# Optimization experiments

Hardware: AMD Instinct MI355X
Metric: run time of the kernel (lower is better)

## Reference

```python
import jax, jax.numpy as jnp
import numpy as np

NEG_SLOPE = 0.2


def _gcn_conv(x, edge_index, W, b):
    # Standard GCNConv: y = D^-1/2 (A + I) D^-1/2 (x W) + b
    N = x.shape[0]
    loop = jnp.arange(N, dtype=edge_index.dtype)
    src = jnp.concatenate([edge_index[0], loop])  # [E+N]
    dst = jnp.concatenate([edge_index[1], loop])  # [E+N]
    deg = jax.ops.segment_sum(jnp.ones_like(dst, dtype=x.dtype), dst, num_segments=N)
    dinv = jnp.where(deg > 0, jax.lax.rsqrt(deg), 0.0)
    norm = dinv[src] * dinv[dst]                  # [E+N]
    h = x @ W                                     # [N, out] dense GEMM
    msg = h[src] * norm[:, None]                  # irregular gather, [E+N, out]
    agg = jax.ops.segment_sum(msg, dst, num_segments=N)  # irregular scatter
    return agg + b


def setup_inputs() -> dict:
    key = jax.random.key(0)
    ks = jax.random.split(key, 5)
    N, E, d_in, d_hid = 50000, 800000, 256, 512
    s = lambda fan_in, fan_out: np.sqrt(6.0 / (fan_in + fan_out))
    return {
        "x": jax.random.normal(ks[0], (N, d_in), dtype=jnp.float32),
        "edge_index": jax.random.randint(ks[1], (2, E), 0, N, dtype=jnp.int64),
        "W_gcn": jax.random.uniform(ks[2], (d_in, d_hid), jnp.float32, -s(d_in, d_hid), s(d_in, d_hid)),
        "b_gcn": jnp.zeros((d_hid,), jnp.float32),
        "W2": jax.random.uniform(ks[3], (d_hid, d_hid), jnp.float32, -s(d_hid, d_hid), s(d_hid, d_hid)),
        "b2": jnp.zeros((d_hid,), jnp.float32),
        "W_out": jax.random.uniform(ks[4], (d_hid, 1), jnp.float32, -s(d_hid, 1), s(d_hid, 1)),
        "b_out": jnp.zeros((1,), jnp.float32),
    }


def reference(x, edge_index, W_gcn, b_gcn, W2, b2, W_out, b_out):
    h = _gcn_conv(x, edge_index, W_gcn, b_gcn)           # [N, 512]
    h = jax.nn.leaky_relu(h, NEG_SLOPE)
    h = jax.nn.leaky_relu(h @ W2 + b2, NEG_SLOPE)        # [N, 512]
    return h @ W_out + b_out                             # [N, 1]
```

## Files before the change

### kernel.cpp

```cpp
#include <hip/hip_runtime.h>

#define D_IN  256
#define D_HID 512
#define NEG_SLOPE 0.2f
#define SCAN_CHUNK 2048

typedef __attribute__((ext_vector_type(8))) short short8;
typedef __attribute__((ext_vector_type(4))) float floatx4;

__device__ __forceinline__ unsigned short f2bf(float f) {
    unsigned int u = __float_as_uint(f);
    u += 0x7fffu + ((u >> 16) & 1u);
    return (unsigned short)(u >> 16);
}
__device__ __forceinline__ float bf2f(unsigned short u) {
    return __uint_as_float(((unsigned int)u) << 16);
}

__device__ __forceinline__ int eidx(const void* ei, long pos, int is64) {
    return is64 ? (int)((const long long*)ei)[pos] : ((const int*)ei)[pos];
}

__global__ __launch_bounds__(256) void k_init(int* __restrict__ deg, int N,
                                              const unsigned int* __restrict__ ei,
                                              int npairs, int* flag,
                                              const float* __restrict__ b_out,
                                              float* __restrict__ out,
                                              const float* __restrict__ Wa,
                                              unsigned short* __restrict__ Wat,
                                              const float* __restrict__ Wb,
                                              unsigned short* __restrict__ Wbt) {
    __shared__ float tl[64][65];
    int b = blockIdx.x;
    if (b < 96) {
        const float* W; unsigned short* Wt; int K, Nc, tk, tn;
        if (b < 32) { W = Wa; Wt = Wat; K = 256; Nc = 512; tk = b & 3; tn = b >> 2; }
        else { b -= 32; W = Wb; Wt = Wbt; K = 512; Nc = 512; tk = b & 7; tn = b >> 3; }
        int k0 = tk * 64, n0 = tn * 64;
        int c = threadIdx.x & 63;
        int r0 = threadIdx.x >> 6;
#pragma unroll
        for (int i = 0; i < 16; ++i) {
            int r = r0 + i * 4;
            tl[r][c] = W[(long)(k0 + r) * Nc + n0 + c];
        }
        __syncthreads();
#pragma unroll
        for (int i = 0; i < 16; ++i) {
            int r = r0 + i * 4;
            Wt[(long)(n0 + r) * K + k0 + c] = f2bf(tl[c][r]);
        }
        return;
    }
    if (b == 96) {
        __shared__ int nz;
        if (threadIdx.x == 0) nz = 0;
        __syncthreads();
        for (int p = threadIdx.x; p < npairs; p += blockDim.x)
            if (ei[2 * p + 1] != 0) nz = 1;
        __syncthreads();
        if (threadIdx.x == 0) *flag = nz ? 0 : 1;
    }
    int t = (b - 96) * 256 + threadIdx.x;
    if (t < N) { deg[t] = 0; out[t] = b_out[0]; }
}

__global__ void k_deg_count(const void* __restrict__ ei, const int* __restrict__ flag,
                            int* __restrict__ deg, int E) {
    int e = blockIdx.x * blockDim.x + threadIdx.x;
    if (e < E) atomicAdd(&deg[eidx(ei, (long)E + e, *flag)], 1);
}

__global__ __launch_bounds__(256) void k_scan1(const int* __restrict__ deg,
                                               int* __restrict__ bsum, int N) {
    int base = blockIdx.x * SCAN_CHUNK;
    int hi = min(base + SCAN_CHUNK, N);
    int s = 0;
    for (int i = base + threadIdx.x; i < hi; i += 256) s += deg[i];
#pragma unroll
    for (int off = 32; off > 0; off >>= 1) s += __shfl_down(s, off, 64);
    __shared__ int lds[4];
    if ((threadIdx.x & 63) == 0) lds[threadIdx.x >> 6] = s;
    __syncthreads();
    if (threadIdx.x == 0) bsum[blockIdx.x] = lds[0] + lds[1] + lds[2] + lds[3];
}

__global__ __launch_bounds__(256) void k_scan23(const int* __restrict__ deg,
                                                const int* __restrict__ bsum, int NB,
                                                int* __restrict__ offs,
                                                int* __restrict__ cursor,
                                                float* __restrict__ dinv, int N) {
    __shared__ int lds[256];
    int t = threadIdx.x;
    int bbase = 0;
    for (int i = 0; i < NB; ++i) bbase += (i < blockIdx.x) ? bsum[i] : 0;
    if (blockIdx.x == NB - 1 && t == 0) offs[N] = bbase + bsum[NB - 1];
    int base = blockIdx.x * SCAN_CHUNK;
    int lo = base + t * 8;
    int v[8], s = 0;
#pragma unroll
    for (int j = 0; j < 8; ++j) {
        int i = lo + j;
        v[j] = (i < N) ? deg[i] : 0;
        s += v[j];
    }
    lds[t] = s;
    __syncthreads();
    for (int d = 1; d < 256; d <<= 1) {
        int add = (t >= d) ? lds[t - d] : 0;
        __syncthreads();
        lds[t] += add;
        __syncthreads();
    }
    int run = bbase + ((t > 0) ? lds[t - 1] : 0);
#pragma unroll
    for (int j = 0; j < 8; ++j) {
        int i = lo + j;
        if (i < N) {
            offs[i] = run; cursor[i] = run;
            dinv[i] = rsqrtf(1.0f + (float)v[j]);
            run += v[j];
        }
    }
}

__global__ __launch_bounds__(256) void k_prefill(const float* __restrict__ x,
                                                 const float* __restrict__ dinv,
                                                 unsigned short* __restrict__ xb,
                                                 const void* __restrict__ ei,
                                                 const int* __restrict__ flag,
                                                 int* __restrict__ cursor,
                                                 int* __restrict__ esrc,
                                                 int N, int E, int PB) {
    if ((int)blockIdx.x < PB) {
        long t = (long)blockIdx.x * 256 + threadIdx.x;
        long total = (long)N * D_IN / 4;
        if (t >= total) return;
        int row = (int)(t >> 6);
        float s = dinv[row];
        float4 v = *(const float4*)(x + t * 4);
        ushort4 o;
        o.x = f2bf(v.x * s); o.y = f2bf(v.y * s); o.z = f2bf(v.z * s); o.w = f2bf(v.w * s);
        *(ushort4*)(xb + t * 4) = o;
        return;
    }
    int e = (blockIdx.x - PB) * 256 + threadIdx.x;
    if (e >= E) return;
    int is64 = *flag;
    int s = eidx(ei, e, is64), d = eidx(ei, (long)E + e, is64);
    int pos = atomicAdd(&cursor[d], 1);
    esrc[pos] = s;
}

__global__ __launch_bounds__(256) void k_gather(const unsigned short* __restrict__ xb,
                                                const int* __restrict__ offs,
                                                const int* __restrict__ esrc,
                                                const float* __restrict__ dinv,
                                                unsigned short* __restrict__ aggb, int N) {
    int node = blockIdx.x * 4 + (threadIdx.x >> 6);
    if (node >= N) return;
    int lane = threadIdx.x & 63;
    int half = lane >> 5;
    int colofs = (lane & 31) * 8;
    const unsigned short* xbc = xb + colofs;
    float di = dinv[node];

    float a[8];
    {
        short8 v = *(const short8*)(xbc + (long)node * D_IN);
#pragma unroll
        for (int j = 0; j < 8; ++j)
            a[j] = (half == 0) ? bf2f((unsigned short)v[j]) : 0.f;
    }

    int beg = offs[node], end = offs[node + 1];
    int e = beg;
    for (; e + 8 <= end; e += 8) {
        int s0 = esrc[e + half];
        int s1 = esrc[e + 2 + half];
        int s2 = esrc[e + 4 + half];
        int s3 = esrc[e + 6 + half];
        short8 u0 = *(const short8*)(xbc + (long)s0 * D_IN);
        short8 u1 = *(const short8*)(xbc + (long)s1 * D_IN);
        short8 u2 = *(const short8*)(xbc + (long)s2 * D_IN);
        short8 u3 = *(const short8*)(xbc + (long)s3 * D_IN);
#pragma unroll
        for (int j = 0; j < 8; ++j) {
            float t0 = bf2f((unsigned short)u0[j]) + bf2f((unsigned short)u1[j]);
            float t1 = bf2f((unsigned short)u2[j]) + bf2f((unsigned short)u3[j]);
            a[j] += t0 + t1;
        }
    }
    for (; e < end; e += 2) {
        int j0 = e + half;
        int jj = (j0 < end) ? j0 : end - 1;
        int s = esrc[jj];
        float w = (j0 < end) ? 1.f : 0.f;
        short8 u = *(const short8*)(xbc + (long)s * D_IN);
#pragma unroll
        for (int j = 0; j < 8; ++j)
            a[j] += w * bf2f((unsigned short)u[j]);
    }

#pragma unroll
    for (int j = 0; j < 8; ++j) a[j] += __shfl_xor(a[j], 32, 64);

    if (half == 0) {
        short8 o;
#pragma unroll
        for (int j = 0; j < 8; ++j) o[j] = (short)f2bf(a[j] * di);
        *(short8*)(aggb + (long)node * D_IN + colofs) = o;
    }
}

__device__ __forceinline__ void async_cp16(const unsigned short* gp, unsigned short* lp) {
    __builtin_amdgcn_global_load_lds((const __attribute__((address_space(1))) void*)gp,
                                     (__attribute__((address_space(3))) void*)lp, 16, 0, 0);
}

__device__ __forceinline__ void stage_sw64(const unsigned short* src, int strideK,
                                           int rowMax, unsigned short* lds, int tid) {
#pragma unroll
    for (int rr = 0; rr < 4; ++rr) {
        int c = rr * 256 + tid;
        int row = c >> 3;
        int ci = (c & 7) ^ (row & 7);
        if (row > rowMax) row = rowMax;
        async_cp16(src + (long)row * strideK + ci * 8, lds + c * 8);
    }
}

__device__ __forceinline__ bool map_block(int b, int M, int& m0, int& n0) {
    int x = b & 7, slot = b >> 3;
    int mt = x + 8 * (slot >> 2);
    m0 = mt * 128; n0 = (slot & 3) * 128;
    return m0 < M;
}

__global__ __launch_bounds__(256) void k_gemm_bf16(const unsigned short* __restrict__ A,
                                                   const unsigned short* __restrict__ Bt,
                                                   const float* __restrict__ bias,
                                                   unsigned short* __restrict__ C,
                                                   int M, int K) {
    __shared__ __align__(16) unsigned short As[2][128 * 64];
    __shared__ __align__(16) unsigned short Bs[2][128 * 64];
    __shared__ __align__(16) unsigned short Ep[32 * 128];
    const int tid  = threadIdx.x;
    const int lane = tid & 63, wave = tid >> 6;
    int m0, n0;
    if (!map_block(blockIdx.x, M, m0, n0)) return;
    const int r = lane & 15, q = lane >> 4;
    const int xv = r & 7;
    const int wm = (wave & 1) * 64, wn = (wave >> 1) * 64;
    const int band = wm >> 6;
    const int rmA = M - 1 - m0;
    const unsigned short* Ab = A + (long)m0 * K;
    const unsigned short* Bb = Bt + (long)n0 * K;

    floatx4 acc[4][4];
#pragma unroll
    for (int i = 0; i < 4; ++i)
#pragma unroll
        for (int j = 0; j < 4; ++j) acc[i][j] = (floatx4){0.f, 0.f, 0.f, 0.f};

    const int nt = K >> 6;
    stage_sw64(Ab, K, rmA, As[0], tid);
    stage_sw64(Bb, K, 127, Bs[0], tid);
    __syncthreads();
    for (int t = 0; t < nt; ++t) {
        const int cur = t & 1;
        if (t + 1 < nt) {
            stage_sw64(Ab + (t + 1) * 64, K, rmA, As[cur ^ 1], tid);
            stage_sw64(Bb + (t + 1) * 64, K, 127, Bs[cur ^ 1], tid);
        }
#pragma unroll
        for (int s = 0; s < 2; ++s) {
            int slotbase = s * 4 + q;
            short8 af[4], bf[4];
#pragma unroll
            for (int i = 0; i < 4; ++i)
                af[i] = *(const short8*)(As[cur] + (wm + i * 16 + r) * 64 + (slotbase ^ xv) * 8);
#pragma unroll
            for (int j = 0; j < 4; ++j)
                bf[j] = *(const short8*)(Bs[cur] + (wn + j * 16 + r) * 64 + (slotbase ^ xv) * 8);
#pragma unroll
            for (int i = 0; i < 4; ++i)
#pragma unroll
                for (int j = 0; j < 4; ++j)
                    acc[i][j] = __builtin_amdgcn_mfma_f32_16x16x32_bf16(af[i], bf[j], acc[i][j], 0, 0, 0);
        }
        __syncthreads();
    }

    float bv[4];
#pragma unroll
    for (int j = 0; j < 4; ++j) bv[j] = bias[n0 + wn + j * 16 + r];

#pragma unroll
    for (int i = 0; i < 4; ++i) {
#pragma unroll
        for (int j = 0; j < 4; ++j) {
#pragma unroll
            for (int t2 = 0; t2 < 4; ++t2) {
                float v = acc[i][j][t2] + bv[j];
                v = v > 0.f ? v : NEG_SLOPE * v;
                Ep[(band * 16 + q * 4 + t2) * 128 + wn + j * 16 + r] = f2bf(v);
            }
        }
        __syncthreads();
#pragma unroll
        for (int rr = 0; rr < 2; ++rr) {
            int c = rr * 256 + tid;
            int lrow = c >> 4, ccol = c & 15;
            int grow = m0 + (lrow >> 4) * 64 + i * 16 + (lrow & 15);
            if (grow < M) {
                short8 v = *(const short8*)(Ep + lrow * 128 + ccol * 8);
                *(short8*)(C + (long)grow * D_HID + n0 + ccol * 8) = v;
            }
        }
        __syncthreads();
    }
}

__global__ __launch_bounds__(256) void k_gemm2f(const unsigned short* __restrict__ A,
                                                const unsigned short* __restrict__ Bt,
                                                const float* __restrict__ bias,
                                                const float* __restrict__ wout,
                                                float* __restrict__ out,
                                                int M, int K) {
    __shared__ __align__(16) unsigned short As[2][128 * 64];
    __shared__ __align__(16) unsigned short Bs[2][128 * 64];
    const int tid  = threadIdx.x;
    const int lane = tid & 63, wave = tid >> 6;
    int m0, n0;
    if (!map_block(blockIdx.x, M, m0, n0)) return;
    const int r = lane & 15, q = lane >> 4;
    const int xv = r & 7;
    const int wm = (wave & 1) * 64, wn = (wave >> 1) * 64;
    const int rmA = M - 1 - m0;
    const unsigned short* Ab = A + (long)m0 * K;
    const unsigned short* Bb = Bt + (long)n0 * K;

    floatx4 acc[4][4];
#pragma unroll
    for (int i = 0; i < 4; ++i)
#pragma unroll
        for (int j = 0; j < 4; ++j) acc[i][j] = (floatx4){0.f, 0.f, 0.f, 0.f};

    const int nt = K >> 6;
    stage_sw64(Ab, K, rmA, As[0], tid);
    stage_sw64(Bb, K, 127, Bs[0], tid);
    __syncthreads();
    for (int t = 0; t < nt; ++t) {
        const int cur = t & 1;
        if (t + 1 < nt) {
            stage_sw64(Ab + (t + 1) * 64, K, rmA, As[cur ^ 1], tid);
            stage_sw64(Bb + (t + 1) * 64, K, 127, Bs[cur ^ 1], tid);
        }
#pragma unroll
        for (int s = 0; s < 2; ++s) {
            int slotbase = s * 4 + q;
            short8 af[4], bf[4];
#pragma unroll
            for (int i = 0; i < 4; ++i)
                af[i] = *(const short8*)(As[cur] + (wm + i * 16 + r) * 64 + (slotbase ^ xv) * 8);
#pragma unroll
            for (int j = 0; j < 4; ++j)
                bf[j] = *(const short8*)(Bs[cur] + (wn + j * 16 + r) * 64 + (slotbase ^ xv) * 8);
#pragma unroll
            for (int i = 0; i < 4; ++i)
#pragma unroll
                for (int j = 0; j < 4; ++j)
                    acc[i][j] = __builtin_amdgcn_mfma_f32_16x16x32_bf16(af[i], bf[j], acc[i][j], 0, 0, 0);
        }
        __syncthreads();
    }

    float bv[4], wv[4];
#pragma unroll
    for (int j = 0; j < 4; ++j) {
        int col = n0 + wn + j * 16 + r;
        bv[j] = bias[col];
        wv[j] = wout[col];
    }
#pragma unroll
    for (int i = 0; i < 4; ++i) {
#pragma unroll
        for (int t2 = 0; t2 < 4; ++t2) {
            float p = 0.f;
#pragma unroll
            for (int j = 0; j < 4; ++j) {
                float v = acc[i][j][t2] + bv[j];
                v = v > 0.f ? v : NEG_SLOPE * v;
                p += v * wv[j];
            }
            p += __shfl_xor(p, 8, 64);
            p += __shfl_xor(p, 4, 64);
            p += __shfl_xor(p, 2, 64);
            p += __shfl_xor(p, 1, 64);
            if (r == 0) {
                int row = m0 + wm + i * 16 + q * 4 + t2;
                if (row < M) atomicAdd(&out[row], p);
            }
        }
    }
}

extern "C" void kernel_launch(void* const* d_in, const int* in_sizes, int n_in,
                              void* d_out, int out_size, void* d_ws, size_t ws_size,
                              hipStream_t stream) {
    const float* x     = (const float*)d_in[0];
    const void*  ei    = d_in[1];
    const float* W_gcn = (const float*)d_in[2];
    const float* b_gcn = (const float*)d_in[3];
    const float* W2    = (const float*)d_in[4];
    const float* b2    = (const float*)d_in[5];
    const float* W_out = (const float*)d_in[6];
    const float* b_out = (const float*)d_in[7];
    float* out = (float*)d_out;

    const int N = in_sizes[0] / D_IN;
    const int E = in_sizes[1] / 2;
    const int NB = (N + SCAN_CHUNK - 1) / SCAN_CHUNK;

    char* w = (char*)d_ws;
    size_t off = 0;
    auto alloc = [&](size_t bytes) { char* p = w + off; off = (off + bytes + 255) & ~(size_t)255; return p; };
    int*            flag   = (int*)alloc(256);
    float*          dinv   = (float*)alloc((size_t)N * 4);
    int*            deg_i  = (int*)alloc((size_t)N * 4);
    int*            offs   = (int*)alloc((size_t)(N + 1) * 4);
    int*            cursor = (int*)alloc((size_t)N * 4);
    int*            bsum   = (int*)alloc((size_t)NB * 4);
    int*            esrc   = (int*)alloc((size_t)(E + 16) * 4);
    unsigned short* xb     = (unsigned short*)alloc((size_t)N * D_IN * 2);
    unsigned short* aggb   = (unsigned short*)alloc((size_t)N * D_IN * 2);
    unsigned short* h1     = (unsigned short*)alloc((size_t)N * D_HID * 2);
    unsigned short* Wgt    = (unsigned short*)alloc((size_t)D_IN * D_HID * 2);
    unsigned short* W2t    = (unsigned short*)alloc((size_t)D_HID * D_HID * 2);

    int npairs = E < 2048 ? E : 2048;
    int init_blocks = 96 + (N + 255) / 256;
    k_init<<<init_blocks, 256, 0, stream>>>(deg_i, N, (const unsigned int*)ei,
                                            npairs, flag, b_out, out,
                                            W_gcn, Wgt, W2, W2t);

    k_deg_count<<<(E + 255) / 256, 256, 0, stream>>>(ei, flag, deg_i, E);
    k_scan1<<<NB, 256, 0, stream>>>(deg_i, bsum, N);
    k_scan23<<<NB, 256, 0, stream>>>(deg_i, bsum, NB, offs, cursor, dinv, N);

    int PB = (int)(((long)N * D_IN / 4 + 255) / 256);
    int FB = (E + 255) / 256;
    k_prefill<<<PB + FB, 256, 0, stream>>>(x, dinv, xb, ei, flag, cursor, esrc, N, E, PB);

    k_gather<<<(N + 3) / 4, 256, 0, stream>>>(xb, offs, esrc, dinv, aggb, N);

    int mtiles = (N + 127) / 128;
    int gblocks = ((mtiles + 7) / 8) * 8 * 4;
    k_gemm_bf16<<<gblocks, 256, 0, stream>>>(aggb, Wgt, b_gcn, h1, N, D_IN);
    k_gemm2f<<<gblocks, 256, 0, stream>>>(h1, W2t, b2, W_out, out, N, D_HID);
}
```

Baseline: 336.7 us.

## Build CSR from atomic ranks and apply source normalization inside the gather

```diff
diff --git a/kernel.cpp b/kernel.cpp
--- a/kernel.cpp
+++ b/kernel.cpp
@@ -21,7 +21,9 @@
     return is64 ? (int)((const long long*)ei)[pos] : ((const int*)ei)[pos];
 }
 
-__global__ __launch_bounds__(256) void k_init(int* __restrict__ deg, int N,
+__global__ __launch_bounds__(256) void k_init(const float* __restrict__ x,
+                                              unsigned short* __restrict__ xb,
+                                              int* __restrict__ deg, int N,
                                               const unsigned int* __restrict__ ei,
                                               int npairs, int* flag,
                                               const float* __restrict__ b_out,
@@ -29,7 +31,8 @@
                                               const float* __restrict__ Wa,
                                               unsigned short* __restrict__ Wat,
                                               const float* __restrict__ Wb,
-                                              unsigned short* __restrict__ Wbt) {
+                                              unsigned short* __restrict__ Wbt,
+                                              long xthreads) {
     __shared__ float tl[64][65];
     int b = blockIdx.x;
     if (b < 96) {
@@ -61,14 +64,21 @@
         __syncthreads();
         if (threadIdx.x == 0) *flag = nz ? 0 : 1;
     }
-    int t = (b - 96) * 256 + threadIdx.x;
+    long t = (long)(b - 96) * 256 + threadIdx.x;
+    if (t < xthreads) {
+        long i = t * 4;
+        float4 v = *(const float4*)(x + i);
+        ushort4 o;
+        o.x = f2bf(v.x); o.y = f2bf(v.y); o.z = f2bf(v.z); o.w = f2bf(v.w);
+        *(ushort4*)(xb + i) = o;
+    }
     if (t < N) { deg[t] = 0; out[t] = b_out[0]; }
 }
 
 __global__ void k_deg_count(const void* __restrict__ ei, const int* __restrict__ flag,
-                            int* __restrict__ deg, int E) {
+                            int* __restrict__ deg, int* __restrict__ rank, int E) {
     int e = blockIdx.x * blockDim.x + threadIdx.x;
-    if (e < E) atomicAdd(&deg[eidx(ei, (long)E + e, *flag)], 1);
+    if (e < E) rank[e] = atomicAdd(&deg[eidx(ei, (long)E + e, *flag)], 1);
 }
 
 __global__ __launch_bounds__(256) void k_scan1(const int* __restrict__ deg,
@@ -88,7 +98,6 @@
 __global__ __launch_bounds__(256) void k_scan23(const int* __restrict__ deg,
                                                 const int* __restrict__ bsum, int NB,
                                                 int* __restrict__ offs,
-                                                int* __restrict__ cursor,
                                                 float* __restrict__ dinv, int N) {
     __shared__ int lds[256];
     int t = threadIdx.x;
@@ -117,39 +126,21 @@
     for (int j = 0; j < 8; ++j) {
         int i = lo + j;
         if (i < N) {
-            offs[i] = run; cursor[i] = run;
+            offs[i] = run;
             dinv[i] = rsqrtf(1.0f + (float)v[j]);
             run += v[j];
         }
     }
 }
 
-__global__ __launch_bounds__(256) void k_prefill(const float* __restrict__ x,
-                                                 const float* __restrict__ dinv,
-                                                 unsigned short* __restrict__ xb,
-                                                 const void* __restrict__ ei,
-                                                 const int* __restrict__ flag,
-                                                 int* __restrict__ cursor,
-                                                 int* __restrict__ esrc,
-                                                 int N, int E, int PB) {
-    if ((int)blockIdx.x < PB) {
-        long t = (long)blockIdx.x * 256 + threadIdx.x;
-        long total = (long)N * D_IN / 4;
-        if (t >= total) return;
-        int row = (int)(t >> 6);
-        float s = dinv[row];
-        float4 v = *(const float4*)(x + t * 4);
-        ushort4 o;
-        o.x = f2bf(v.x * s); o.y = f2bf(v.y * s); o.z = f2bf(v.z * s); o.w = f2bf(v.w * s);
-        *(ushort4*)(xb + t * 4) = o;
-        return;
-    }
-    int e = (blockIdx.x - PB) * 256 + threadIdx.x;
+__global__ void k_fill(const void* __restrict__ ei, const int* __restrict__ flag,
+                       const int* __restrict__ offs, const int* __restrict__ rank,
+                       int* __restrict__ esrc, int E) {
+    int e = blockIdx.x * blockDim.x + threadIdx.x;
     if (e >= E) return;
     int is64 = *flag;
     int s = eidx(ei, e, is64), d = eidx(ei, (long)E + e, is64);
-    int pos = atomicAdd(&cursor[d], 1);
-    esrc[pos] = s;
+    esrc[offs[d] + rank[e]] = s;
 }
 
 __global__ __launch_bounds__(256) void k_gather(const unsigned short* __restrict__ xb,
@@ -158,19 +149,19 @@
                                                 const float* __restrict__ dinv,
                                                 unsigned short* __restrict__ aggb, int N) {
     int node = blockIdx.x * 4 + (threadIdx.x >> 6);
+    int lane = threadIdx.x & 63;
     if (node >= N) return;
-    int lane = threadIdx.x & 63;
     int half = lane >> 5;
-    int colofs = (lane & 31) * 8;
-    const unsigned short* xbc = xb + colofs;
+    int li   = lane & 31;
+    int colofs = li * 8;
     float di = dinv[node];
 
     float a[8];
     {
-        short8 v = *(const short8*)(xbc + (long)node * D_IN);
+        short8 v = *(const short8*)(xb + (long)node * D_IN + colofs);
 #pragma unroll
         for (int j = 0; j < 8; ++j)
-            a[j] = (half == 0) ? bf2f((unsigned short)v[j]) : 0.f;
+            a[j] = (half == 0) ? di * bf2f((unsigned short)v[j]) : 0.f;
     }
 
     int beg = offs[node], end = offs[node + 1];
@@ -180,23 +171,22 @@
         int s1 = esrc[e + 2 + half];
         int s2 = esrc[e + 4 + half];
         int s3 = esrc[e + 6 + half];
-        short8 u0 = *(const short8*)(xbc + (long)s0 * D_IN);
-        short8 u1 = *(const short8*)(xbc + (long)s1 * D_IN);
-        short8 u2 = *(const short8*)(xbc + (long)s2 * D_IN);
-        short8 u3 = *(const short8*)(xbc + (long)s3 * D_IN);
-#pragma unroll
-        for (int j = 0; j < 8; ++j) {
-            float t0 = bf2f((unsigned short)u0[j]) + bf2f((unsigned short)u1[j]);
-            float t1 = bf2f((unsigned short)u2[j]) + bf2f((unsigned short)u3[j]);
-            a[j] += t0 + t1;
-        }
+        float w0 = dinv[s0], w1 = dinv[s1], w2 = dinv[s2], w3 = dinv[s3];
+        short8 u0 = *(const short8*)(xb + (long)s0 * D_IN + colofs);
+        short8 u1 = *(const short8*)(xb + (long)s1 * D_IN + colofs);
+        short8 u2 = *(const short8*)(xb + (long)s2 * D_IN + colofs);
+        short8 u3 = *(const short8*)(xb + (long)s3 * D_IN + colofs);
+#pragma unroll
+        for (int j = 0; j < 8; ++j)
+            a[j] += w0 * bf2f((unsigned short)u0[j]) + w1 * bf2f((unsigned short)u1[j])
+                  + w2 * bf2f((unsigned short)u2[j]) + w3 * bf2f((unsigned short)u3[j]);
     }
     for (; e < end; e += 2) {
         int j0 = e + half;
         int jj = (j0 < end) ? j0 : end - 1;
         int s = esrc[jj];
-        float w = (j0 < end) ? 1.f : 0.f;
-        short8 u = *(const short8*)(xbc + (long)s * D_IN);
+        float w = (j0 < end) ? dinv[s] : 0.f;
+        short8 u = *(const short8*)(xb + (long)s * D_IN + colofs);
 #pragma unroll
         for (int j = 0; j < 8; ++j)
             a[j] += w * bf2f((unsigned short)u[j]);
@@ -430,8 +420,8 @@
     float*          dinv   = (float*)alloc((size_t)N * 4);
     int*            deg_i  = (int*)alloc((size_t)N * 4);
     int*            offs   = (int*)alloc((size_t)(N + 1) * 4);
-    int*            cursor = (int*)alloc((size_t)N * 4);
     int*            bsum   = (int*)alloc((size_t)NB * 4);
+    int*            rank   = (int*)alloc((size_t)(E + 16) * 4);
     int*            esrc   = (int*)alloc((size_t)(E + 16) * 4);
     unsigned short* xb     = (unsigned short*)alloc((size_t)N * D_IN * 2);
     unsigned short* aggb   = (unsigned short*)alloc((size_t)N * D_IN * 2);
@@ -440,18 +430,16 @@
     unsigned short* W2t    = (unsigned short*)alloc((size_t)D_HID * D_HID * 2);
 
     int npairs = E < 2048 ? E : 2048;
-    int init_blocks = 96 + (N + 255) / 256;
-    k_init<<<init_blocks, 256, 0, stream>>>(deg_i, N, (const unsigned int*)ei,
+    long xthreads = (long)N * D_IN / 4;
+    int init_blocks = 96 + (int)((xthreads + 255) / 256);
+    k_init<<<init_blocks, 256, 0, stream>>>(x, xb, deg_i, N, (const unsigned int*)ei,
                                             npairs, flag, b_out, out,
-                                            W_gcn, Wgt, W2, W2t);
-
-    k_deg_count<<<(E + 255) / 256, 256, 0, stream>>>(ei, flag, deg_i, E);
+                                            W_gcn, Wgt, W2, W2t, xthreads);
+
+    k_deg_count<<<(E + 255) / 256, 256, 0, stream>>>(ei, flag, deg_i, rank, E);
     k_scan1<<<NB, 256, 0, stream>>>(deg_i, bsum, N);
-    k_scan23<<<NB, 256, 0, stream>>>(deg_i, bsum, NB, offs, cursor, dinv, N);
-
-    int PB = (int)(((long)N * D_IN / 4 + 255) / 256);
-    int FB = (E + 255) / 256;
-    k_prefill<<<PB + FB, 256, 0, stream>>>(x, dinv, xb, ei, flag, cursor, esrc, N, E, PB);
+    k_scan23<<<NB, 256, 0, stream>>>(deg_i, bsum, NB, offs, dinv, N);
+    k_fill<<<(E + 255) / 256, 256, 0, stream>>>(ei, flag, offs, rank, esrc, E);
 
     k_gather<<<(N + 3) / 4, 256, 0, stream>>>(xb, offs, esrc, dinv, aggb, N);
 
```

After: 296.4 us. 1.14x faster.
